# Performance work log

Measured on AMD Instinct MI355X. Metric: run time of the kernel, lower is better.

The kernel has to match this reference:

```python
import jax, jax.numpy as jnp
import numpy as np

MAX_ANGLES = 6
SCALES = 2
BN_EPS = 1e-5


def _gauss(k):
    # Gaussian filter init used by WaveletTransform1D (kernel_size k, sigma=k/4)
    xs = np.arange(k, dtype=np.float32) - k // 2
    w = np.exp(-xs ** 2 / (2.0 * (k / 4.0) ** 2)).astype(np.float32)
    return jnp.asarray((w / w.sum()).reshape(1, 1, k))


def setup_inputs():
    key = jax.random.key(0)
    ks = jax.random.split(key, 8)
    B, C, H, W = 8, 64, 128, 128
    return {
        "x": jax.random.normal(ks[0], (B, C, H, W), jnp.float32),
        "lin1_w": jax.random.normal(ks[1], (32, C * 16), jnp.float32) * 0.02,
        "lin1_b": jnp.zeros((32,), jnp.float32),
        "lin2_w": jax.random.normal(ks[2], (MAX_ANGLES, 32), jnp.float32) * 0.02,
        "lin2_b": jnp.zeros((MAX_ANGLES,), jnp.float32),
        "wf0": _gauss(3),
        "wf1": _gauss(5),
        "fuse_w": jax.random.normal(ks[3], (C, C * SCALES), jnp.float32) * 0.05,
        "fuse_b": jax.random.normal(ks[4], (C,), jnp.float32) * 0.05,
        "bn_gamma": jnp.ones((C,), jnp.float32),
        "bn_beta": jnp.zeros((C,), jnp.float32),
        "bn_mean": jnp.zeros((C,), jnp.float32),
        "bn_var": jnp.ones((C,), jnp.float32),
    }


def _grid_sample(img, grid):
    # torch F.grid_sample, bilinear, align_corners=True, padding_mode='zeros'
    N, C, H, W = img.shape
    ix = (grid[..., 0] + 1.0) * 0.5 * (W - 1)  # (N,Hg,Wg)
    iy = (grid[..., 1] + 1.0) * 0.5 * (H - 1)
    x0 = jnp.floor(ix)
    y0 = jnp.floor(iy)
    wx = ix - x0
    wy = iy - y0

    def gather(xi, yi):
        valid = (xi >= 0) & (xi <= W - 1) & (yi >= 0) & (yi <= H - 1)
        xc = jnp.clip(xi, 0, W - 1).astype(jnp.int32)
        yc = jnp.clip(yi, 0, H - 1).astype(jnp.int32)
        v = jax.vmap(lambda im, yy, xx: im[:, yy, xx])(img, yc, xc)  # (N,C,Hg,Wg)
        return v * valid[:, None, :, :].astype(img.dtype)

    v00 = gather(x0, y0)
    v01 = gather(x0 + 1, y0)
    v10 = gather(x0, y0 + 1)
    v11 = gather(x0 + 1, y0 + 1)
    return (v00 * ((1 - wx) * (1 - wy))[:, None]
            + v01 * (wx * (1 - wy))[:, None]
            + v10 * ((1 - wx) * wy)[:, None]
            + v11 * (wx * wy)[:, None])


def _interp1d(x, Lout):
    # F.interpolate mode='linear', align_corners=False, over last axis
    Lin = x.shape[-1]
    real = jnp.clip((jnp.arange(Lout, dtype=jnp.float32) + 0.5) * (Lin / Lout) - 0.5, 0.0, Lin - 1.0)
    i0 = jnp.floor(real).astype(jnp.int32)
    i1 = jnp.minimum(i0 + 1, Lin - 1)
    w = real - i0
    return x[..., i0] * (1.0 - w) + x[..., i1] * w


def _interp_last_ac(x, Lout):
    # linear interp over last axis, align_corners=True
    Lin = x.shape[-1]
    if Lin == Lout:
        return x
    pos = jnp.arange(Lout, dtype=jnp.float32) * ((Lin - 1) / (Lout - 1))
    i0 = jnp.floor(pos).astype(jnp.int32)
    i1 = jnp.minimum(i0 + 1, Lin - 1)
    w = pos - i0
    return x[..., i0] * (1.0 - w) + x[..., i1] * w


def _avgpool1(x):
    L = x.shape[-1]
    return x[..., : (L // 2) * 2].reshape(x.shape[:-1] + (L // 2, 2)).mean(-1)


def _conv1(sig, w):
    # sig (N,1,L), w (1,1,k), 'same' padding cross-correlation (matches torch Conv1d)
    k = w.shape[-1]
    return jax.lax.conv_general_dilated(sig, w, (1,), [(k // 2, k // 2)],
                                        dimension_numbers=("NCH", "OIH", "NCH"))


def reference(x, lin1_w, lin1_b, lin2_w, lin2_b, wf0, wf1, fuse_w, fuse_b,
              bn_gamma, bn_beta, bn_mean, bn_var):
    B, C, H, W = x.shape
    K = MAX_ANGLES
    # --- AnglePredictor: adaptive avg pool 4x4 (H,W divisible by 4) + MLP ---
    pooled = x.reshape(B, C, 4, H // 4, 4, W // 4).mean(axis=(3, 5))  # (B,C,4,4)
    feat = pooled.reshape(B, C * 16)
    h = jax.nn.relu(feat @ lin1_w.T + lin1_b)
    off = (h @ lin2_w.T + lin2_b) * 30.0
    base = jnp.linspace(0.0, 180.0, K)
    angles = jnp.sort(jnp.clip(base[None, :] + off, 0.0, 180.0), axis=1)  # (B,K)
    # --- RadonTransform: per-angle rotation grid + grid_sample + sum over W ---
    xs = jnp.linspace(-1.0, 1.0, W)
    ys = jnp.linspace(-1.0, 1.0, H)
    yc, xc = jnp.meshgrid(ys, xs, indexing="ij")
    th = angles * (jnp.pi / 180.0)
    co = jnp.cos(th)[:, :, None, None]
    si = jnp.sin(th)[:, :, None, None]
    gx = xc[None, None] * co + yc[None, None] * si
    gy = -xc[None, None] * si + yc[None, None] * co
    grid = jnp.stack([gx, gy], axis=-1).reshape(B * K, H, W, 2)
    xexp = jnp.broadcast_to(x[:, None], (B, K, C, H, W)).reshape(B * K, C, H, W)
    rotated = _grid_sample(xexp, grid)          # (B*K,C,H,W)
    sig = rotated.sum(axis=3)                   # (B*K,C,H) == sinogram permuted
    # --- WaveletTransform1D (2 scales, L=H=128 > 4) ---
    N = B * K
    c0 = _conv1(sig.reshape(N * C, 1, H), wf0).reshape(N, C, H)
    cur = _avgpool1(sig)                        # (N,C,H//2)
    L2 = H // 2
    f1 = _conv1(cur.reshape(N * C, 1, L2), wf1)
    u1 = _interp1d(_avgpool1(f1), L2).reshape(N, C, L2)
    c1 = _interp1d(u1, H)                       # resized to target length H
    coeffs = jnp.stack([c0, c1], axis=2)        # (N,C,SCALES,H)
    wav = coeffs.reshape(B, K, C, SCALES, H).transpose(0, 2, 4, 3, 1)  # (B,C,H,S,K)
    combined = wav.reshape(B, C * SCALES, H, K)  # matches torch .view on contiguous
    # --- bilinear align_corners=True resize (H,K)->(H,W), separable ---
    combined = _interp_last_ac(combined, W)
    combined = _interp_last_ac(combined.swapaxes(-1, -2), H).swapaxes(-1, -2)
    # --- fusion: 1x1 conv + BatchNorm(eval) + ReLU ---
    out = jnp.einsum("oc,bchw->bohw", fuse_w, combined) + fuse_b[None, :, None, None]
    scale = (bn_gamma / jnp.sqrt(bn_var + BN_EPS))[None, :, None, None]
    out = (out - bn_mean[None, :, None, None]) * scale + bn_beta[None, :, None, None]
    return jax.nn.relu(out)
```

## Files before the change

### kernel.cpp

```cpp
#include <hip/hip_runtime.h>
#include <math.h>

#define BB 8
#define CC 64
#define HH 128
#define WW 128
#define KK 6

#define FEAT_OFF 0
#define COEF_OFF 8192

#define STR  133
#define NROW 132
#define IMG_SZ (NROW * STR)

__global__ __launch_bounds__(256) void k_pool(const float* __restrict__ x,
                                              float* __restrict__ ws) {
    int bc = blockIdx.x;
    int b = bc >> 6, c = bc & 63;
    int t = threadIdx.x;
    __shared__ float pool_l[16];
    if (t < 16) pool_l[t] = 0.f;
    __syncthreads();
    const float4* img4 = (const float4*)(x + (size_t)bc * 16384);
    float acc[4] = {0.f, 0.f, 0.f, 0.f};
    int cb = (t & 31) >> 3;
    #pragma unroll
    for (int r = 0; r < 16; ++r) {
        float4 v = img4[r * 256 + t];
        acc[r >> 2] += (v.x + v.y) + (v.z + v.w);
    }
    #pragma unroll
    for (int rb = 0; rb < 4; ++rb)
        atomicAdd(&pool_l[rb * 4 + cb], acc[rb]);
    __syncthreads();
    if (t < 16)
        ws[FEAT_OFF + b * 1024 + c * 16 + t] = pool_l[t] * (1.0f / 1024.0f);
}

#define SAMPLE(RR, CC, ACC) do {                                   \
    float fr_ = floorf(RR), fc_ = floorf(CC);                      \
    float wr_ = (RR) - fr_, wc_ = (CC) - fc_;                      \
    const float* q_ = base2 + (int)fmaf(fr_, 133.f, fc_);          \
    float q0_ = q_[0],   q1_ = q_[1];                \
    float q2_ = q_[STR], q3_ = q_[STR + 1];          \
    float t0_ = fmaf(wc_, q1_ - q0_, q0_);                         \
    float t1_ = fmaf(wc_, q3_ - q2_, q2_);                         \
    ACC += fmaf(wr_, t1_ - t0_, t0_);                              \
} while (0)

__global__ __launch_bounds__(256) void k_radon(const float* __restrict__ x,
                                               const float* __restrict__ lin1_w,
                                               const float* __restrict__ lin1_b,
                                               const float* __restrict__ lin2_w,
                                               const float* __restrict__ lin2_b,
                                               const float* __restrict__ wf0,
                                               const float* __restrict__ wf1,
                                               float* __restrict__ ws) {
    int bc = blockIdx.x;
    int b = bc >> 6, c = bc & 63;
    int t = threadIdx.x;
    __shared__ float img[IMG_SZ];
    __shared__ float sigl[768];
    __shared__ float feat_l[8 * 132];
    __shared__ float h_l[32];
    __shared__ float ang_l[6], ang_s[6];
    __shared__ float co_l[6], si_l[6];

    for (int i = t; i < 2 * STR; i += 256) {
        img[i] = 0.f;
        img[130 * STR + i] = 0.f;
    }
    if (t < 128) {
        float* r = img + (t + 2) * STR;
        r[0] = 0.f; r[1] = 0.f; r[130] = 0.f; r[131] = 0.f; r[132] = 0.f;
    }
    const float4* src4 = (const float4*)(x + (size_t)bc * 16384);
    for (int i = t; i < 4096; i += 256) {
        float4 v = src4[i];
        float* d = img + ((i >> 5) + 2) * STR + ((i & 31) << 2) + 2;
        d[0] = v.x; d[1] = v.y; d[2] = v.z; d[3] = v.w;
    }
    const float* feat = ws + FEAT_OFF + b * 1024;
    for (int i = t; i < 1024; i += 256)
        feat_l[(i >> 7) * 132 + (i & 127)] = feat[i];
    __syncthreads();
    {
        int m = t >> 3, part = t & 7;
        const float4* wrow = (const float4*)(lin1_w + m * 1024 + part * 128);
        const float4* frow = (const float4*)(feat_l + part * 132);
        float acc = 0.f;
        #pragma unroll 8
        for (int i = 0; i < 32; ++i) {
            float4 wv = wrow[i], fv = frow[i];
            acc = fmaf(wv.x, fv.x, acc); acc = fmaf(wv.y, fv.y, acc);
            acc = fmaf(wv.z, fv.z, acc); acc = fmaf(wv.w, fv.w, acc);
        }
        acc += __shfl_xor(acc, 1);
        acc += __shfl_xor(acc, 2);
        acc += __shfl_xor(acc, 4);
        if (part == 0) h_l[m] = fmaxf(acc + lin1_b[m], 0.f);
    }
    __syncthreads();
    if (t < 6) {
        float a = lin2_b[t];
        #pragma unroll
        for (int i = 0; i < 32; ++i) a = fmaf(h_l[i], lin2_w[t * 32 + i], a);
        a = 36.0f * (float)t + a * 30.0f;
        ang_l[t] = fminf(fmaxf(a, 0.f), 180.f);
    }
    __syncthreads();
    if (t == 0) {
        float v[6];
        #pragma unroll
        for (int i = 0; i < 6; ++i) v[i] = ang_l[i];
        for (int i = 1; i < 6; ++i) {
            float key = v[i]; int j = i - 1;
            while (j >= 0 && v[j] > key) { v[j + 1] = v[j]; --j; }
            v[j + 1] = key;
        }
        #pragma unroll
        for (int i = 0; i < 6; ++i) ang_s[i] = v[i];
    }
    __syncthreads();
    if (t < 6) {
        float th = ang_s[t] * (3.14159265358979323846f / 180.0f);
        co_l[t] = cosf(th);
        si_l[t] = sinf(th);
    }
    __syncthreads();

    const float* base2 = img + 2 * STR + 2;

    for (int p = t; p < 768; p += 256) {
        int k = p >> 7, h = p & 127;
        float co = co_l[k], si = si_l[k];
        float yc = fmaf((float)h, 2.0f / 127.0f, -1.0f);
        float ix0 = (fmaf(yc, si, -co) + 1.0f) * 63.5f;
        float iy0 = (fmaf(yc, co,  si) + 1.0f) * 63.5f;

        float ic = 1.0f / co, is = 1.0f / (-si);
        float a1 = (-1.0f - ix0) * ic, a2 = (128.0f - ix0) * ic;
        float b1 = (-1.0f - iy0) * is, b2 = (128.0f - iy0) * is;
        float wlo = fmaxf(fminf(a1, a2), fminf(b1, b2));
        float whi = fminf(fmaxf(a1, a2), fmaxf(b1, b2));
        int wA = max((int)ceilf(fmaxf(fminf(wlo, 200.f), -200.f)), 0);
        int wB = min((int)floorf(fmaxf(fminf(whi, 200.f), -200.f)), 127);
        while (wA <= wB) {
            float cx = fmaf((float)wA, co, ix0), ry = fmaf((float)wA, -si, iy0);
            if (cx >= -1.f && cx <= 128.f && ry >= -1.f && ry <= 128.f) break;
            ++wA;
        }
        while (wB >= wA) {
            float cx = fmaf((float)wB, co, ix0), ry = fmaf((float)wB, -si, iy0);
            if (cx >= -1.f && cx <= 128.f && ry >= -1.f && ry <= 128.f) break;
            --wB;
        }

        int n = wB - wA + 1;
        float rr0 = fmaf((float)wA, -si, iy0);
        float cc0 = fmaf((float)wA,  co, ix0);
        float rr1 = rr0 - si, cc1 = cc0 + co;
        float rr2 = rr1 - si, cc2 = cc1 + co;
        float rr3 = rr2 - si, cc3 = cc2 + co;
        float si4 = 4.0f * si, co4 = 4.0f * co;
        float a0 = 0.f, aa1 = 0.f, aa2 = 0.f, a3 = 0.f;
        int i = n;
        while (i >= 4) {
            SAMPLE(rr0, cc0, a0);
            SAMPLE(rr1, cc1, aa1);
            SAMPLE(rr2, cc2, aa2);
            SAMPLE(rr3, cc3, a3);
            rr0 -= si4; cc0 += co4;
            rr1 -= si4; cc1 += co4;
            rr2 -= si4; cc2 += co4;
            rr3 -= si4; cc3 += co4;
            i -= 4;
        }
        if (i > 0) SAMPLE(rr0, cc0, a0);
        if (i > 1) SAMPLE(rr1, cc1, aa1);
        if (i > 2) SAMPLE(rr2, cc2, aa2);
        sigl[p] = (a0 + aa1) + (aa2 + a3);
    }
    __syncthreads();

    float* cur = img;
    float* f1  = img + 384;
    float* p1  = img + 768;
    float* u1  = img + 960;
    float g0 = wf0[0], g1 = wf0[1], g2 = wf0[2];

    for (int p = t; p < 768; p += 256) {
        int k = p >> 7, h = p & 127;
        const float* s = sigl + k * 128;
        float sm1 = (h > 0)   ? s[h - 1] : 0.f;
        float sp1 = (h < 127) ? s[h + 1] : 0.f;
        float c0 = sm1 * g0 + s[h] * g1 + sp1 * g2;
        ws[COEF_OFF + (((b * 6 + k) * 64 + c) * 2 + 0) * 128 + h] = c0;
    }
    for (int q = t; q < 384; q += 256) {
        int k = q >> 6, l = q & 63;
        cur[q] = (sigl[k * 128 + 2 * l] + sigl[k * 128 + 2 * l + 1]) * 0.5f;
    }
    __syncthreads();

    float w10 = wf1[0], w11 = wf1[1], w12 = wf1[2], w13 = wf1[3], w14 = wf1[4];
    for (int q = t; q < 384; q += 256) {
        int k = q >> 6, l = q & 63;
        const float* cu = cur + k * 64;
        float a = cu[l] * w12;
        a += (l >= 2)  ? cu[l - 2] * w10 : 0.f;
        a += (l >= 1)  ? cu[l - 1] * w11 : 0.f;
        a += (l <= 62) ? cu[l + 1] * w13 : 0.f;
        a += (l <= 61) ? cu[l + 2] * w14 : 0.f;
        f1[q] = a;
    }
    __syncthreads();

    for (int q = t; q < 192; q += 256) {
        int k = q >> 5, m = q & 31;
        p1[q] = (f1[k * 64 + 2 * m] + f1[k * 64 + 2 * m + 1]) * 0.5f;
    }
    __syncthreads();

    for (int q = t; q < 384; q += 256) {
        int k = q >> 6, l = q & 63;
        float real = fminf(fmaxf(0.5f * (float)l - 0.25f, 0.f), 31.f);
        int i0 = (int)real;
        int i1 = min(i0 + 1, 31);
        float wv = real - (float)i0;
        u1[q] = p1[k * 32 + i0] * (1.f - wv) + p1[k * 32 + i1] * wv;
    }
    __syncthreads();

    for (int p = t; p < 768; p += 256) {
        int k = p >> 7, h = p & 127;
        float real = fminf(fmaxf(0.5f * (float)h - 0.25f, 0.f), 63.f);
        int i0 = (int)real;
        int i1 = min(i0 + 1, 63);
        float wv = real - (float)i0;
        float c1 = u1[k * 64 + i0] * (1.f - wv) + u1[k * 64 + i1] * wv;
        ws[COEF_OFF + (((b * 6 + k) * 64 + c) * 2 + 1) * 128 + h] = c1;
    }
}

__global__ __launch_bounds__(256) void k_fuseout(const float* __restrict__ fuse_w,
                                                 const float* __restrict__ fuse_b,
                                                 const float* __restrict__ bn_gamma,
                                                 const float* __restrict__ bn_beta,
                                                 const float* __restrict__ bn_mean,
                                                 const float* __restrict__ bn_var,
                                                 const float* __restrict__ ws,
                                                 float* __restrict__ out) {
    int blk = blockIdx.x;
    int b = blk >> 5, oh = (blk >> 4) & 1, j = blk & 15;
    int t = threadIdx.x;
    __shared__ float M_l[6 * 128 * 8];
    __shared__ float W_l[32 * 129];
    __shared__ float S_l[32 * 8 * 6];

    for (int i = t; i < 6144; i += 256) {
        int x4 = i & 3, half = (i >> 2) & 1, s = (i >> 3) & 1;
        int cc = (i >> 4) & 63, k = i >> 10;
        int hp = half * 64 + 4 * j + x4;
        int c2 = 2 * cc + half;
        int h2p = 2 * x4 + s;
        M_l[(k * 128 + c2) * 8 + h2p] =
            ws[COEF_OFF + (((b * 6 + k) * 64 + cc) * 2 + s) * 128 + hp];
    }
    for (int i = t; i < 4096; i += 256) {
        int op = i >> 7, c2 = i & 127;
        W_l[op * 129 + c2] = fuse_w[(oh * 32 + op) * 128 + c2];
    }
    __syncthreads();

    {
        int op = t >> 3, h2p = t & 7;
        float acc[6] = {0.f, 0.f, 0.f, 0.f, 0.f, 0.f};
        const float* wrow = W_l + op * 129;
        #pragma unroll 4
        for (int c2 = 0; c2 < 128; ++c2) {
            float wv = wrow[c2];
            const float* m = M_l + c2 * 8 + h2p;
            #pragma unroll
            for (int k = 0; k < 6; ++k)
                acc[k] = fmaf(wv, m[k * 1024], acc[k]);
        }
        int o = oh * 32 + op;
        float scale = bn_gamma[o] * rsqrtf(bn_var[o] + 1e-5f);
        float shift = (fuse_b[o] - bn_mean[o]) * scale + bn_beta[o];
        float* srow = S_l + (op * 8 + h2p) * 6;
        #pragma unroll
        for (int k = 0; k < 6; ++k)
            srow[k] = fmaf(acc[k], scale, shift);
    }
    __syncthreads();

    for (int it = 0; it < 128; ++it) {
        int flat = it * 256 + t;
        int w = flat & 127, row = flat >> 7;
        float pos = (float)w * (5.0f / 127.0f);
        int i0 = min((int)pos, 5);
        int i1 = min(i0 + 1, 5);
        float tt = pos - (float)i0;
        const float* srow = S_l + row * 6;
        float val = srow[i0] * (1.f - tt) + srow[i1] * tt;
        int o = oh * 32 + (row >> 3);
        int h2 = 8 * j + (row & 7);
        out[(((b * 64 + o) * 128) + h2) * 128 + w] = fmaxf(val, 0.f);
    }
}

extern "C" void kernel_launch(void* const* d_in, const int* in_sizes, int n_in,
                              void* d_out, int out_size, void* d_ws, size_t ws_size,
                              hipStream_t stream) {
    const float* x        = (const float*)d_in[0];
    const float* lin1_w   = (const float*)d_in[1];
    const float* lin1_b   = (const float*)d_in[2];
    const float* lin2_w   = (const float*)d_in[3];
    const float* lin2_b   = (const float*)d_in[4];
    const float* wf0      = (const float*)d_in[5];
    const float* wf1      = (const float*)d_in[6];
    const float* fuse_w   = (const float*)d_in[7];
    const float* fuse_b   = (const float*)d_in[8];
    const float* bn_gamma = (const float*)d_in[9];
    const float* bn_beta  = (const float*)d_in[10];
    const float* bn_mean  = (const float*)d_in[11];
    const float* bn_var   = (const float*)d_in[12];
    float* ws  = (float*)d_ws;
    float* out = (float*)d_out;

    hipLaunchKernelGGL(k_pool,    dim3(BB * CC), dim3(256), 0, stream, x, ws);
    hipLaunchKernelGGL(k_radon,   dim3(BB * CC), dim3(256), 0, stream,
                       x, lin1_w, lin1_b, lin2_w, lin2_b, wf0, wf1, ws);
    hipLaunchKernelGGL(k_fuseout, dim3(256),     dim3(256), 0, stream,
                       fuse_w, fuse_b, bn_gamma, bn_beta, bn_mean, bn_var,
                       ws, out);
}
```

Before: 170.6 us.

## Double radon block threads and split remaining ray sums across thread pairs

The radon kernel goes from 256 to 512 threads per block. Each of the first 512 projection lines gets its own thread, and the last 256 lines are each split in half across a thread pair and combined with a shuffle. The old layout gave each thread three serial line integrals; the new one shortens the per-thread critical path to about 1.5 lines. In exchange it uses more registers per block, and launch bounds of (512,4) may cap registers and limit occupancy given the large shared-memory image per block.

```diff
diff --git a/kernel.cpp b/kernel.cpp
--- a/kernel.cpp
+++ b/kernel.cpp
@@ -49,14 +49,64 @@
     ACC += fmaf(wr_, t1_ - t0_, t0_);                              \
 } while (0)
 
-__global__ __launch_bounds__(256) void k_radon(const float* __restrict__ x,
-                                               const float* __restrict__ lin1_w,
-                                               const float* __restrict__ lin1_b,
-                                               const float* __restrict__ lin2_w,
-                                               const float* __restrict__ lin2_b,
-                                               const float* __restrict__ wf0,
-                                               const float* __restrict__ wf1,
-                                               float* __restrict__ ws) {
+__device__ __forceinline__ void line_bounds(float co, float si, float ix0,
+                                            float iy0, int& wA, int& wB) {
+    float ic = 1.0f / co, is = 1.0f / (-si);
+    float a1 = (-1.0f - ix0) * ic, a2 = (128.0f - ix0) * ic;
+    float b1 = (-1.0f - iy0) * is, b2 = (128.0f - iy0) * is;
+    float wlo = fmaxf(fminf(a1, a2), fminf(b1, b2));
+    float whi = fminf(fmaxf(a1, a2), fmaxf(b1, b2));
+    wA = max((int)ceilf(fmaxf(fminf(wlo, 200.f), -200.f)), 0);
+    wB = min((int)floorf(fmaxf(fminf(whi, 200.f), -200.f)), 127);
+    while (wA <= wB) {
+        float cx = fmaf((float)wA, co, ix0), ry = fmaf((float)wA, -si, iy0);
+        if (cx >= -1.f && cx <= 128.f && ry >= -1.f && ry <= 128.f) break;
+        ++wA;
+    }
+    while (wB >= wA) {
+        float cx = fmaf((float)wB, co, ix0), ry = fmaf((float)wB, -si, iy0);
+        if (cx >= -1.f && cx <= 128.f && ry >= -1.f && ry <= 128.f) break;
+        --wB;
+    }
+}
+
+__device__ __forceinline__ float radon_line(const float* base2, float co,
+                                            float si, float ix0, float iy0,
+                                            int wA, int wB) {
+    int n = wB - wA + 1;
+    float rr0 = fmaf((float)wA, -si, iy0);
+    float cc0 = fmaf((float)wA,  co, ix0);
+    float rr1 = rr0 - si, cc1 = cc0 + co;
+    float rr2 = rr1 - si, cc2 = cc1 + co;
+    float rr3 = rr2 - si, cc3 = cc2 + co;
+    float si4 = 4.0f * si, co4 = 4.0f * co;
+    float a0 = 0.f, a1 = 0.f, a2 = 0.f, a3 = 0.f;
+    int i = n;
+    while (i >= 4) {
+        SAMPLE(rr0, cc0, a0);
+        SAMPLE(rr1, cc1, a1);
+        SAMPLE(rr2, cc2, a2);
+        SAMPLE(rr3, cc3, a3);
+        rr0 -= si4; cc0 += co4;
+        rr1 -= si4; cc1 += co4;
+        rr2 -= si4; cc2 += co4;
+        rr3 -= si4; cc3 += co4;
+        i -= 4;
+    }
+    if (i > 0) SAMPLE(rr0, cc0, a0);
+    if (i > 1) SAMPLE(rr1, cc1, a1);
+    if (i > 2) SAMPLE(rr2, cc2, a2);
+    return (a0 + a1) + (a2 + a3);
+}
+
+__global__ __launch_bounds__(512, 4) void k_radon(const float* __restrict__ x,
+                                                  const float* __restrict__ lin1_w,
+                                                  const float* __restrict__ lin1_b,
+                                                  const float* __restrict__ lin2_w,
+                                                  const float* __restrict__ lin2_b,
+                                                  const float* __restrict__ wf0,
+                                                  const float* __restrict__ wf1,
+                                                  float* __restrict__ ws) {
     int bc = blockIdx.x;
     int b = bc >> 6, c = bc & 63;
     int t = threadIdx.x;
@@ -67,7 +117,7 @@
     __shared__ float ang_l[6], ang_s[6];
     __shared__ float co_l[6], si_l[6];
 
-    for (int i = t; i < 2 * STR; i += 256) {
+    for (int i = t; i < 2 * STR; i += 512) {
         img[i] = 0.f;
         img[130 * STR + i] = 0.f;
     }
@@ -76,16 +126,16 @@
         r[0] = 0.f; r[1] = 0.f; r[130] = 0.f; r[131] = 0.f; r[132] = 0.f;
     }
     const float4* src4 = (const float4*)(x + (size_t)bc * 16384);
-    for (int i = t; i < 4096; i += 256) {
+    for (int i = t; i < 4096; i += 512) {
         float4 v = src4[i];
         float* d = img + ((i >> 5) + 2) * STR + ((i & 31) << 2) + 2;
         d[0] = v.x; d[1] = v.y; d[2] = v.z; d[3] = v.w;
     }
     const float* feat = ws + FEAT_OFF + b * 1024;
-    for (int i = t; i < 1024; i += 256)
+    for (int i = t; i < 1024; i += 512)
         feat_l[(i >> 7) * 132 + (i & 127)] = feat[i];
     __syncthreads();
-    {
+    if (t < 256) {
         int m = t >> 3, part = t & 7;
         const float4* wrow = (const float4*)(lin1_w + m * 1024 + part * 128);
         const float4* frow = (const float4*)(feat_l + part * 132);
@@ -132,55 +182,31 @@
 
     const float* base2 = img + 2 * STR + 2;
 
-    for (int p = t; p < 768; p += 256) {
-        int k = p >> 7, h = p & 127;
+    {
+        int p = t, k = p >> 7, h = p & 127;
         float co = co_l[k], si = si_l[k];
         float yc = fmaf((float)h, 2.0f / 127.0f, -1.0f);
         float ix0 = (fmaf(yc, si, -co) + 1.0f) * 63.5f;
         float iy0 = (fmaf(yc, co,  si) + 1.0f) * 63.5f;
-
-        float ic = 1.0f / co, is = 1.0f / (-si);
-        float a1 = (-1.0f - ix0) * ic, a2 = (128.0f - ix0) * ic;
-        float b1 = (-1.0f - iy0) * is, b2 = (128.0f - iy0) * is;
-        float wlo = fmaxf(fminf(a1, a2), fminf(b1, b2));
-        float whi = fminf(fmaxf(a1, a2), fmaxf(b1, b2));
-        int wA = max((int)ceilf(fmaxf(fminf(wlo, 200.f), -200.f)), 0);
-        int wB = min((int)floorf(fmaxf(fminf(whi, 200.f), -200.f)), 127);
-        while (wA <= wB) {
-            float cx = fmaf((float)wA, co, ix0), ry = fmaf((float)wA, -si, iy0);
-            if (cx >= -1.f && cx <= 128.f && ry >= -1.f && ry <= 128.f) break;
-            ++wA;
-        }
-        while (wB >= wA) {
-            float cx = fmaf((float)wB, co, ix0), ry = fmaf((float)wB, -si, iy0);
-            if (cx >= -1.f && cx <= 128.f && ry >= -1.f && ry <= 128.f) break;
-            --wB;
-        }
-
-        int n = wB - wA + 1;
-        float rr0 = fmaf((float)wA, -si, iy0);
-        float cc0 = fmaf((float)wA,  co, ix0);
-        float rr1 = rr0 - si, cc1 = cc0 + co;
-        float rr2 = rr1 - si, cc2 = cc1 + co;
-        float rr3 = rr2 - si, cc3 = cc2 + co;
-        float si4 = 4.0f * si, co4 = 4.0f * co;
-        float a0 = 0.f, aa1 = 0.f, aa2 = 0.f, a3 = 0.f;
-        int i = n;
-        while (i >= 4) {
-            SAMPLE(rr0, cc0, a0);
-            SAMPLE(rr1, cc1, aa1);
-            SAMPLE(rr2, cc2, aa2);
-            SAMPLE(rr3, cc3, a3);
-            rr0 -= si4; cc0 += co4;
-            rr1 -= si4; cc1 += co4;
-            rr2 -= si4; cc2 += co4;
-            rr3 -= si4; cc3 += co4;
-            i -= 4;
-        }
-        if (i > 0) SAMPLE(rr0, cc0, a0);
-        if (i > 1) SAMPLE(rr1, cc1, aa1);
-        if (i > 2) SAMPLE(rr2, cc2, aa2);
-        sigl[p] = (a0 + aa1) + (aa2 + a3);
+        int wA, wB;
+        line_bounds(co, si, ix0, iy0, wA, wB);
+        sigl[p] = radon_line(base2, co, si, ix0, iy0, wA, wB);
+    }
+    {
+        int p = 512 + (t >> 1), k = p >> 7, h = p & 127;
+        int half = t & 1;
+        float co = co_l[k], si = si_l[k];
+        float yc = fmaf((float)h, 2.0f / 127.0f, -1.0f);
+        float ix0 = (fmaf(yc, si, -co) + 1.0f) * 63.5f;
+        float iy0 = (fmaf(yc, co,  si) + 1.0f) * 63.5f;
+        int wA, wB;
+        line_bounds(co, si, ix0, iy0, wA, wB);
+        int mid = wA + ((wB - wA + 1) >> 1);
+        int sA = half ? mid : wA;
+        int sB = half ? wB : (mid - 1);
+        float a = radon_line(base2, co, si, ix0, iy0, sA, sB);
+        a += __shfl_xor(a, 1);
+        if (half == 0) sigl[p] = a;
     }
     __syncthreads();
 
@@ -190,7 +216,7 @@
     float* u1  = img + 960;
     float g0 = wf0[0], g1 = wf0[1], g2 = wf0[2];
 
-    for (int p = t; p < 768; p += 256) {
+    for (int p = t; p < 768; p += 512) {
         int k = p >> 7, h = p & 127;
         const float* s = sigl + k * 128;
         float sm1 = (h > 0)   ? s[h - 1] : 0.f;
@@ -198,14 +224,14 @@
         float c0 = sm1 * g0 + s[h] * g1 + sp1 * g2;
         ws[COEF_OFF + (((b * 6 + k) * 64 + c) * 2 + 0) * 128 + h] = c0;
     }
-    for (int q = t; q < 384; q += 256) {
+    for (int q = t; q < 384; q += 512) {
         int k = q >> 6, l = q & 63;
         cur[q] = (sigl[k * 128 + 2 * l] + sigl[k * 128 + 2 * l + 1]) * 0.5f;
     }
     __syncthreads();
 
     float w10 = wf1[0], w11 = wf1[1], w12 = wf1[2], w13 = wf1[3], w14 = wf1[4];
-    for (int q = t; q < 384; q += 256) {
+    for (int q = t; q < 384; q += 512) {
         int k = q >> 6, l = q & 63;
         const float* cu = cur + k * 64;
         float a = cu[l] * w12;
@@ -217,13 +243,13 @@
     }
     __syncthreads();
 
-    for (int q = t; q < 192; q += 256) {
+    for (int q = t; q < 192; q += 512) {
         int k = q >> 5, m = q & 31;
         p1[q] = (f1[k * 64 + 2 * m] + f1[k * 64 + 2 * m + 1]) * 0.5f;
     }
     __syncthreads();
 
-    for (int q = t; q < 384; q += 256) {
+    for (int q = t; q < 384; q += 512) {
         int k = q >> 6, l = q & 63;
         float real = fminf(fmaxf(0.5f * (float)l - 0.25f, 0.f), 31.f);
         int i0 = (int)real;
@@ -233,7 +259,7 @@
     }
     __syncthreads();
 
-    for (int p = t; p < 768; p += 256) {
+    for (int p = t; p < 768; p += 512) {
         int k = p >> 7, h = p & 127;
         float real = fminf(fmaxf(0.5f * (float)h - 0.25f, 0.f), 63.f);
         int i0 = (int)real;
@@ -331,7 +357,7 @@
     float* out = (float*)d_out;
 
     hipLaunchKernelGGL(k_pool,    dim3(BB * CC), dim3(256), 0, stream, x, ws);
-    hipLaunchKernelGGL(k_radon,   dim3(BB * CC), dim3(256), 0, stream,
+    hipLaunchKernelGGL(k_radon,   dim3(BB * CC), dim3(512), 0, stream,
                        x, lin1_w, lin1_b, lin2_w, lin2_b, wf0, wf1, ws);
     hipLaunchKernelGGL(k_fuseout, dim3(256),     dim3(256), 0, stream,
                        fuse_w, fuse_b, bn_gamma, bn_beta, bn_mean, bn_var,
```

Measured after the change: 169.3 us. Within noise of the previous version (-0.8%).
